# Kernel tuning notes

Measured on AMD Instinct MI355X. Metric: run time of the kernel, lower is better.

Reference implementation:

```python
import jax, jax.numpy as jnp
from jax import lax
import numpy as np
import math

B, L, D = 2, 1536, 1024
H = 8
C = 2 * D          # d_wide
DPH = C // H       # 256, dim_per_head
K = 4              # causal conv kernel size


def _ln(x, w, b=None, eps=1e-5):
    mu = jnp.mean(x, -1, keepdims=True)
    var = jnp.mean((x - mu) ** 2, -1, keepdims=True)
    y = (x - mu) * lax.rsqrt(var + eps) * w
    return y + b if b is not None else y


def setup_inputs() -> dict:
    key = jax.random.key(0)
    ks = jax.random.split(key, 8)
    x = jax.random.normal(ks[0], (B, L, D), jnp.float32)
    ln_w = jnp.ones((D,), jnp.float32)
    ln_b = jnp.zeros((D,), jnp.float32)
    w1 = jax.random.normal(ks[1], (4 * D, D), jnp.float32) * math.sqrt(2.0 / 5.0 / D)
    b1 = jnp.zeros((4 * D,), jnp.float32)
    conv_w = jax.random.normal(ks[2], (C, C, K), jnp.float32) * (1.0 / math.sqrt(C * K))
    conv_b = jnp.zeros((C,), jnp.float32)
    skip = jnp.ones((C,), jnp.float32)
    wqk = jax.random.normal(ks[3], (H, DPH, 2 * DPH), jnp.float32) * (1.0 / math.sqrt(DPH))
    bqk = jnp.zeros((H, 2 * DPH), jnp.float32)
    wv = jax.random.normal(ks[4], (H, DPH, DPH), jnp.float32) * (1.0 / math.sqrt(DPH))
    bv = jnp.zeros((H, DPH), jnp.float32)
    wif = jnp.zeros((2 * H, 3 * C), jnp.float32)  # zero-init per source
    bif = jnp.concatenate([jax.random.normal(ks[5], (H,), jnp.float32) * 0.1,
                           jnp.linspace(3.0, 6.0, H, dtype=jnp.float32)])
    hn_w = jnp.ones((DPH,), jnp.float32)
    w2 = jax.random.normal(ks[6], (D, C), jnp.float32) * (2.0 / 24.0 / math.sqrt(D))
    b2 = jnp.zeros((D,), jnp.float32)
    return {"x": x, "ln_w": ln_w, "ln_b": ln_b, "w1": w1, "b1": b1,
            "conv_w": conv_w, "conv_b": conv_b, "skip": skip,
            "wqk": wqk, "bqk": bqk, "wv": wv, "bv": bv,
            "wif": wif, "bif": bif, "hn_w": hn_w, "w2": w2, "b2": b2}


def _causal_conv(x1, conv_w, conv_b):
    # literal translation: permute(1,2,0), left-pad last dim, conv1d, permute(2,0,1)
    t = jnp.transpose(x1, (1, 2, 0))                  # (L, C, B)
    t = jnp.pad(t, ((0, 0), (0, 0), (K - 1, 0)))      # left pad along dim0 of original
    o = lax.conv_general_dilated(t, conv_w, (1,), 'VALID',
                                 dimension_numbers=('NCH', 'OIH', 'NCH'))
    o = o + conv_b[None, :, None]
    return jnp.transpose(o, (2, 0, 1))                # (B, L, C)


def _mlstm_core(qk, v_in, wqk, bqk, wv, bv, wif, bif, hn_w):
    b_, l_, c_ = qk.shape
    qkh = qk.reshape(b_, l_, H, DPH)
    proj = jnp.einsum('blhi,hio->blho', qkh, wqk) + bqk       # (B,L,H,2*DPH)
    q, k = jnp.split(proj, 2, axis=-1)                        # each (B,L,H,DPH)
    v = jnp.einsum('blhi,hio->blho', v_in.reshape(b_, l_, H, DPH), wv) + bv
    qkv = jnp.concatenate([proj, v], axis=-1).reshape(b_, l_, 3 * c_)
    gates = qkv @ wif.T + bif                                 # (B,L,2H)
    i_g, f_g = jnp.split(gates, 2, axis=-1)                   # (B,L,H)
    i_g = jnp.exp(i_g)
    f_c = jnp.cumsum(jax.nn.log_sigmoid(f_g), axis=1)
    fmat = f_c[:, :, None, :] - f_c[:, None, :, :]            # (B,o,i,H)
    mask = jnp.triu(jnp.ones((l_, l_), bool), 1)[None, :, :, None]
    fmat = jnp.where(mask, -jnp.inf, fmat)
    d = fmat + i_g[:, None, :, :]
    m = jnp.max(d, axis=-2, keepdims=True)                    # over i: (B,o,1,H)
    d = jnp.exp(d - m)
    ks_ = k / math.sqrt(DPH)
    c = jnp.einsum('bohd,bihd->boih', q, ks_) * d
    bsum = jnp.sum(c, axis=-2, keepdims=True)                 # (B,o,1,H)
    n = jnp.maximum(jnp.abs(bsum), jnp.exp(-m))
    c = c / n
    h = jnp.einsum('boih,bihd->bohd', c, v)                   # (B,L,H,DPH)
    h = _ln(h, hn_w)                                          # LayerNorm, no bias
    return h.reshape(b_, l_, c_)


def reference(x, ln_w, ln_b, w1, b1, conv_w, conv_b, skip, wqk, bqk, wv, bv,
              wif, bif, hn_w, w2, b2):
    y = _ln(x, ln_w, ln_b) @ w1.T + b1                        # (B,L,4D)
    x1, x2 = jnp.split(y, 2, axis=-1)                         # each (B,L,C)
    qk = jax.nn.silu(_causal_conv(x1, conv_w, conv_b))
    h = _mlstm_core(qk, x1, wqk, bqk, wv, bv, wif, bif, hn_w)
    x1o = h + skip * qk
    xm = x1o * jax.nn.silu(x2)
    return xm @ w2.T + b2 + x
```

## Files before the change

kernel.cpp:

```cpp
#include <hip/hip_runtime.h>

typedef unsigned short u16;
typedef __bf16 bf16x8 __attribute__((ext_vector_type(8)));
typedef float f32x4 __attribute__((ext_vector_type(4)));
typedef unsigned short us8 __attribute__((ext_vector_type(8)));

#define MFMA(a,b,c) __builtin_amdgcn_mfma_f32_16x16x32_bf16((a),(b),(c),0,0,0)
#define DEV __device__ __forceinline__

DEV u16 f2bf(float f){
  unsigned u = __float_as_uint(f);
  u += 0x7fffu + ((u >> 16) & 1u);
  return (u16)(u >> 16);
}
DEV float bf2f(u16 v){ return __uint_as_float(((unsigned)v)<<16); }
DEV float silu_f(float v){ return v / (1.f + __expf(-v)); }
DEV bf16x8 asbf(us8 v){ return __builtin_bit_cast(bf16x8, v); }

__global__ void prep_kernel(const float* __restrict__ w1, const float* __restrict__ w2,
                            const float* __restrict__ wif, const float* __restrict__ conv_w,
                            const float* __restrict__ wqk, const float* __restrict__ wv,
                            u16* __restrict__ w1b, u16* __restrict__ w2b, u16* __restrict__ wifb,
                            u16* __restrict__ cw2, u16* __restrict__ cw3,
                            u16* __restrict__ wqkt, u16* __restrict__ wvt)
{
  const long N0 = 4194304;
  const long N1 = N0 + 2097152;
  const long N2 = N1 + 98304;
  const long N3 = N2 + 4194304;
  const long N4 = N3 + 1048576;
  const long N5 = N4 + 524288;
  long stride = (long)gridDim.x * blockDim.x;
  for (long i = (long)blockIdx.x*blockDim.x + threadIdx.x; i < N5; i += stride) {
    if (i < N0)      { w1b[i] = f2bf(w1[i]); }
    else if (i < N1) { long j = i-N0; w2b[j] = f2bf(w2[j]); }
    else if (i < N2) { long j = i-N1; wifb[j] = f2bf(wif[j]); }
    else if (i < N3) { long j = i-N2; float2 t = *(const float2*)(conv_w + j*4 + 2);
                       cw2[j] = f2bf(t.x); cw3[j] = f2bf(t.y); }
    else if (i < N4) { long j = i-N3; long h=j>>17, r=j&131071, o=r>>8, ii=r&255;
                       wqkt[j] = f2bf(wqk[h*131072 + ii*512 + o]); }
    else             { long j = i-N4; long h=j>>16, o=(j>>8)&255, ii=j&255;
                       wvt[j] = f2bf(wv[h*65536 + ii*256 + o]); }
  }
}

__global__ __launch_bounds__(256) void ln_kernel(const float* __restrict__ x,
        const float* __restrict__ w, const float* __restrict__ b, u16* __restrict__ xn)
{
  int row = blockIdx.x, tid = threadIdx.x;
  const float* xr = x + (long)row*1024;
  float4 v = *(const float4*)(xr + tid*4);
  float s = v.x+v.y+v.z+v.w;
  float q = v.x*v.x+v.y*v.y+v.z*v.z+v.w*v.w;
  #pragma unroll
  for (int off=32; off>=1; off>>=1){ s += __shfl_xor(s,off); q += __shfl_xor(q,off); }
  __shared__ float red[8];
  int wv_ = tid>>6;
  if ((tid&63)==0){ red[wv_*2]=s; red[wv_*2+1]=q; }
  __syncthreads();
  s = red[0]+red[2]+red[4]+red[6];
  q = red[1]+red[3]+red[5]+red[7];
  float mu = s*(1.f/1024.f);
  float var = q*(1.f/1024.f) - mu*mu;
  float rs = rsqrtf(var + 1e-5f);
  int c = tid*4;
  u16 o0 = f2bf((v.x-mu)*rs*w[c+0] + b[c+0]);
  u16 o1 = f2bf((v.y-mu)*rs*w[c+1] + b[c+1]);
  u16 o2 = f2bf((v.z-mu)*rs*w[c+2] + b[c+2]);
  u16 o3 = f2bf((v.w-mu)*rs*w[c+3] + b[c+3]);
  uint2 pk;
  pk.x = (unsigned)o0 | ((unsigned)o1<<16);
  pk.y = (unsigned)o2 | ((unsigned)o3<<16);
  *(uint2*)(xn + (long)row*1024 + c) = pk;
}

__global__ __launch_bounds__(256,2) void gemm_bt(
    const u16* __restrict__ A, long lda, long sAz,
    const u16* __restrict__ A2,
    const u16* __restrict__ Bm, long ldb, long sBz,
    const u16* __restrict__ B2,
    int K1, int Ktot, int convmode,
    const float* __restrict__ bias, long sBiasz,
    int epi,
    float* __restrict__ outf, long ldo, long sOfz,
    u16* __restrict__ outb, long ldob, long sObz,
    const float* __restrict__ resid,
    float* __restrict__ outf2)
{
  __shared__ u16 AsF[4096];
  __shared__ u16 BsF[4096];
  int tid = threadIdx.x;
  int bz = blockIdx.z;
  A += (long)bz*sAz; Bm += (long)bz*sBz;
  const float* biasz = bias ? (bias + (long)bz*sBiasz) : bias;
  u16* outbz = outb ? (outb + (long)bz*sObz) : outb;
  float* outfz = outf ? (outf + (long)bz*sOfz) : outf;
  long am0 = (long)blockIdx.y*128;
  long bn0 = (long)blockIdx.x*128;
  int lane = tid&63, wave = tid>>6, quad = lane>>4, l15 = lane&15;
  int wm = wave>>1, wn = wave&1;
  int kq8 = quad*8;
  int dual = convmode && (bz==1);
  int Kt = dual ? Ktot : K1;
  f32x4 acc[4][4] = {};
  for (int k0=0; k0<Kt; k0+=32) {
    const u16* Ak; const u16* Bk; int kk;
    if (dual){
      if (k0 < K1){ Ak = A; Bk = B2; kk = k0; }
      else        { Ak = A2; Bk = Bm; kk = k0 - K1; }
    } else { Ak = A; Bk = Bm; kk = k0; }
    __syncthreads();
    __builtin_amdgcn_global_load_lds((const __attribute__((address_space(1))) void*)(Ak + (am0 + wave*16 + l15)*lda + kk + kq8),
                                     (__attribute__((address_space(3))) void*)(AsF + wave*512), 16, 0, 0);
    __builtin_amdgcn_global_load_lds((const __attribute__((address_space(1))) void*)(Ak + (am0 + (wave+4)*16 + l15)*lda + kk + kq8),
                                     (__attribute__((address_space(3))) void*)(AsF + (wave+4)*512), 16, 0, 0);
    __builtin_amdgcn_global_load_lds((const __attribute__((address_space(1))) void*)(Bk + (bn0 + wave*16 + l15)*ldb + kk + kq8),
                                     (__attribute__((address_space(3))) void*)(BsF + wave*512), 16, 0, 0);
    __builtin_amdgcn_global_load_lds((const __attribute__((address_space(1))) void*)(Bk + (bn0 + (wave+4)*16 + l15)*ldb + kk + kq8),
                                     (__attribute__((address_space(3))) void*)(BsF + (wave+4)*512), 16, 0, 0);
    __syncthreads();
    bf16x8 af[4], bfr[4];
    #pragma unroll
    for (int t=0;t<4;t++){
      af[t]  = *(const bf16x8*)&AsF[(wm*4+t)*512 + quad*128 + l15*8];
      bfr[t] = *(const bf16x8*)&BsF[(wn*4+t)*512 + quad*128 + l15*8];
    }
    #pragma unroll
    for (int ti=0;ti<4;ti++)
      #pragma unroll
      for (int tj=0;tj<4;tj++)
        acc[ti][tj] = MFMA(af[ti], bfr[tj], acc[ti][tj]);
  }
  #pragma unroll
  for (int ti=0;ti<4;ti++)
  #pragma unroll
  for (int tj=0;tj<4;tj++)
  #pragma unroll
  for (int r=0;r<4;r++){
    long m = am0 + wm*64 + ti*16 + quad*4 + r;
    long n = bn0 + wn*64 + tj*16 + l15;
    float v = acc[ti][tj][r];
    if (epi==1){ outbz[m*ldob+n] = f2bf(v + biasz[n]); }
    else if (epi==2){
      v += biasz[n];
      if (n < 2048) outbz[m*ldob+n] = f2bf(v);
      else outf2[m*2048 + n - 2048] = silu_f(v);
    }
    else if (epi==3){
      v += biasz[n]; v = silu_f(v);
      outfz[m*ldo+n] = v; outbz[m*ldob+n] = f2bf(v);
    }
    else { outfz[m*ldo+n] = v + biasz[n] + resid[m*1024+n]; }
  }
}

__global__ __launch_bounds__(256) void gates_gemm(const u16* __restrict__ qkv,
        const u16* __restrict__ wifb, float* __restrict__ gates)
{
  int tid = threadIdx.x;
  int lane = tid&63, wave = tid>>6, quad = lane>>4, l15 = lane&15;
  long m0 = (long)blockIdx.x*128 + wave*32;
  int ks = blockIdx.y*1536;
  const u16* arow = qkv + (m0 + l15)*6144;
  const u16* brow = wifb + (long)l15*6144;
  f32x4 acc[2] = {};
  for (int k0=ks; k0<ks+1536; k0+=32){
    bf16x8 a0 = *(const bf16x8*)(arow + k0 + quad*8);
    bf16x8 a1 = *(const bf16x8*)(arow + (long)16*6144 + k0 + quad*8);
    bf16x8 bb = *(const bf16x8*)(brow + k0 + quad*8);
    acc[0] = MFMA(a0,bb,acc[0]);
    acc[1] = MFMA(a1,bb,acc[1]);
  }
  #pragma unroll
  for (int mt=0;mt<2;mt++)
  #pragma unroll
  for (int r=0;r<4;r++)
    atomicAdd(&gates[(m0 + mt*16 + quad*4 + r)*16 + l15], acc[mt][r]);
}

__global__ void scan_kernel(const float* __restrict__ gates, const float* __restrict__ bif,
        float* __restrict__ g_arr, float* __restrict__ mg_arr, float* __restrict__ enm)
{
  int bh = blockIdx.x; int b = bh>>3, h = bh&7;
  int lane = threadIdx.x;
  float bi = bif[h], bff = bif[8+h];
  float fl[24], gl[24];
  int l0 = lane*24;
  float s = 0.f;
  #pragma unroll
  for (int j=0;j<24;j++){
    int l = l0+j;
    float f = gates[((long)(b*1536+l))*16 + 8 + h] + bff;
    float ls = fminf(f,0.f) - log1pf(expf(-fabsf(f)));
    fl[j] = ls; s += ls;
  }
  float tot = s;
  for (int off=1; off<64; off<<=1){ float t = __shfl_up(s, off); if (lane>=off) s += t; }
  float fc = s - tot;
  float lm = -INFINITY;
  #pragma unroll
  for (int j=0;j<24;j++){
    int l = l0+j;
    fc += fl[j];
    fl[j] = fc;
    float ir = gates[((long)(b*1536+l))*16 + h] + bi;
    float g = expf(ir) - fc;
    gl[j] = g;
    lm = fmaxf(lm, g);
  }
  float im = lm;
  for (int off=1; off<64; off<<=1){ float t = __shfl_up(im, off); if (lane>=off) im = fmaxf(im,t); }
  float ex = __shfl_up(im, 1);
  if (lane==0) ex = -INFINITY;
  float rm = ex;
  #pragma unroll
  for (int j=0;j<24;j++){
    rm = fmaxf(rm, gl[j]);
    long idx = (long)bh*1536 + l0 + j;
    g_arr[idx] = gl[j];
    mg_arr[idx] = rm;
    enm[idx] = expf(-(fl[j] + rm));
  }
}

__global__ __launch_bounds__(256) void repack_kernel(const u16* __restrict__ qkv,
        u16* __restrict__ qf, u16* __restrict__ kf, u16* __restrict__ vf)
{
  int bh = blockIdx.x, c = blockIdx.y;
  int b = bh>>3, h = bh&7;
  int tid = threadIdx.x;
  long rowb = (long)b*1536 + c*32;
  #pragma unroll
  for (int s4=0; s4<4; s4++){
    int s = s4*256 + tid;
    int n16 = s>>9, kc=(s>>6)&7, l=s&63, quad=l>>4, l15=l&15;
    const u16* src = qkv + (rowb + n16*16 + l15)*6144 + h*768 + kc*32 + quad*8;
    us8 q = *(const us8*)src;
    us8 k = *(const us8*)(src + 256);
    us8 ksc;
    #pragma unroll
    for (int j=0;j<8;j++) ksc[j] = f2bf(bf2f(k[j])*0.0625f);
    int tj = s>>6;
    us8 v;
    #pragma unroll
    for (int j=0;j<8;j++)
      v[j] = qkv[(rowb + quad*8 + j)*6144 + h*768 + 512 + tj*16 + l15];
    long dst = ((long)(bh*48+c))*8192 + (long)s*8;
    *(us8*)(qf+dst) = q;
    *(us8*)(kf+dst) = ksc;
    *(us8*)(vf+dst) = v;
  }
}

__global__ __launch_bounds__(256,2) void attn_kernel(
    const u16* __restrict__ qf, const u16* __restrict__ kf, const u16* __restrict__ vf,
    const float* __restrict__ g_arr, const float* __restrict__ mg_arr,
    const float* __restrict__ enm,
    const float* __restrict__ hn_w, const float* __restrict__ skip,
    const float* __restrict__ qkf, const float* __restrict__ s2,
    u16* __restrict__ xm)
{
  __shared__ u16 pl[4][32][40];
  __shared__ float red[256*36];
  __shared__ float redb[3][32];
  int tid = threadIdx.x;
  int lane = tid&63, wave = tid>>6, quad = lane>>4, l15 = lane&15;
  int bh = blockIdx.x, b = bh>>3, h = bh&7;
  int otile = 47 - blockIdx.y;
  int ow0 = otile*32;
  const u16* qfb = qf + ((long)(bh*48+otile))*8192;
  us8 qreg[2][8];
  #pragma unroll
  for (int mt=0;mt<2;mt++)
    #pragma unroll
    for (int kc=0;kc<8;kc++)
      qreg[mt][kc] = *(const us8*)(qfb + mt*4096 + kc*512 + lane*8);
  float mg[2][4];
  #pragma unroll
  for (int mt=0;mt<2;mt++)
    #pragma unroll
    for (int r=0;r<4;r++)
      mg[mt][r] = mg_arr[(long)bh*1536 + ow0 + mt*16 + quad*4 + r];
  f32x4 accv[2][16] = {};
  float bs[2][4] = {};
  for (int it=wave; it<=otile; it+=4){
    int i0 = it*32;
    const u16* kfb = kf + ((long)(bh*48+it))*8192;
    f32x4 sacc[2][2] = {};
    #pragma unroll
    for (int kc=0;kc<8;kc++){
      bf16x8 b0 = *(const bf16x8*)(kfb + kc*512 + lane*8);
      bf16x8 b1 = *(const bf16x8*)(kfb + 4096 + kc*512 + lane*8);
      sacc[0][0] = MFMA(asbf(qreg[0][kc]), b0, sacc[0][0]);
      sacc[0][1] = MFMA(asbf(qreg[0][kc]), b1, sacc[0][1]);
      sacc[1][0] = MFMA(asbf(qreg[1][kc]), b0, sacc[1][0]);
      sacc[1][1] = MFMA(asbf(qreg[1][kc]), b1, sacc[1][1]);
    }
    #pragma unroll
    for (int nt=0;nt<2;nt++){
      float gi = g_arr[(long)bh*1536 + i0 + nt*16 + l15];
      #pragma unroll
      for (int mt=0;mt<2;mt++)
        #pragma unroll
        for (int r=0;r<4;r++){
          int oi = ow0 + mt*16 + quad*4 + r;
          int ii = i0 + nt*16 + l15;
          float p = (ii <= oi) ? sacc[mt][nt][r]*__expf(gi - mg[mt][r]) : 0.f;
          bs[mt][r] += p;
          pl[wave][mt*16+quad*4+r][nt*16+l15] = f2bf(p);
        }
    }
    const u16* vfb = vf + ((long)(bh*48+it))*8192;
    bf16x8 pa0 = *(const bf16x8*)&pl[wave][l15][quad*8];
    bf16x8 pa1 = *(const bf16x8*)&pl[wave][16+l15][quad*8];
    #pragma unroll
    for (int tj=0;tj<16;tj++){
      bf16x8 vb = *(const bf16x8*)(vfb + tj*512 + lane*8);
      accv[0][tj] = MFMA(pa0, vb, accv[0][tj]);
      accv[1][tj] = MFMA(pa1, vb, accv[1][tj]);
    }
  }
  #pragma unroll
  for (int mt=0;mt<2;mt++)
    #pragma unroll
    for (int r=0;r<4;r++)
      #pragma unroll
      for (int off=1; off<16; off<<=1) bs[mt][r] += __shfl_xor(bs[mt][r], off);
  for (int w=1; w<4; w++){
    if (wave==w){
      #pragma unroll
      for (int mt=0;mt<2;mt++)
        #pragma unroll
        for (int tj=0;tj<16;tj++)
          *(f32x4*)&red[(tj*16+l15)*36 + mt*16 + quad*4] = accv[mt][tj];
      if (l15==0){
        #pragma unroll
        for (int mt=0;mt<2;mt++)
          #pragma unroll
          for (int r=0;r<4;r++)
            redb[w-1][mt*16+quad*4+r] = bs[mt][r];
      }
    }
    __syncthreads();
    if (wave==0){
      #pragma unroll
      for (int mt=0;mt<2;mt++)
        #pragma unroll
        for (int tj=0;tj<16;tj++)
          accv[mt][tj] += *(const f32x4*)&red[(tj*16+l15)*36 + mt*16 + quad*4];
      #pragma unroll
      for (int mt=0;mt<2;mt++)
        #pragma unroll
        for (int r=0;r<4;r++)
          bs[mt][r] += redb[w-1][mt*16+quad*4+r];
    }
    __syncthreads();
  }
  if (wave != 0) return;
  long browg = (long)b*1536;
  #pragma unroll
  for (int mt=0;mt<2;mt++){
    #pragma unroll
    for (int r=0;r<4;r++){
      int row = ow0 + mt*16 + quad*4 + r;
      float s1 = 0.f, sq = 0.f;
      #pragma unroll
      for (int tj=0;tj<16;tj++){ float a = accv[mt][tj][r]; s1 += a; sq += a*a; }
      #pragma unroll
      for (int off=1; off<16; off<<=1){ s1 += __shfl_xor(s1,off); sq += __shfl_xor(sq,off); }
      float nv = fmaxf(fabsf(bs[mt][r]), enm[(long)bh*1536 + row]);
      float inv = 1.f/nv;
      float mu = s1*inv*(1.f/256.f);
      float var = sq*inv*inv*(1.f/256.f) - mu*mu;
      float rs = rsqrtf(var + 1e-5f);
      long rg = browg + row;
      #pragma unroll
      for (int tj=0;tj<16;tj++){
        int col = tj*16 + l15;
        int cc = h*256 + col;
        float y = (accv[mt][tj][r]*inv - mu)*rs*hn_w[col];
        float xv = (y + skip[cc]*qkf[rg*2048 + cc]) * s2[rg*2048 + cc];
        xm[rg*2048 + cc] = f2bf(xv);
      }
    }
  }
}

extern "C" void kernel_launch(void* const* d_in, const int* in_sizes, int n_in,
                              void* d_out, int out_size, void* d_ws, size_t ws_size,
                              hipStream_t stream)
{
  const float* x      = (const float*)d_in[0];
  const float* ln_w   = (const float*)d_in[1];
  const float* ln_b   = (const float*)d_in[2];
  const float* w1     = (const float*)d_in[3];
  const float* b1     = (const float*)d_in[4];
  const float* conv_w = (const float*)d_in[5];
  const float* conv_b = (const float*)d_in[6];
  const float* skip   = (const float*)d_in[7];
  const float* wqk    = (const float*)d_in[8];
  const float* bqk    = (const float*)d_in[9];
  const float* wv     = (const float*)d_in[10];
  const float* bv     = (const float*)d_in[11];
  const float* wif    = (const float*)d_in[12];
  const float* bif    = (const float*)d_in[13];
  const float* hn_w   = (const float*)d_in[14];
  const float* w2     = (const float*)d_in[15];
  const float* b2     = (const float*)d_in[16];
  float* out = (float*)d_out;

  char* p = (char*)d_ws;
  auto alloc = [&](size_t bytes)->void*{ void* r = (void*)p; p += (bytes + 255) & ~(size_t)255; return r; };
  u16* w1b  = (u16*)alloc((size_t)4194304*2);
  u16* w2b  = (u16*)alloc((size_t)2097152*2);
  u16* wifb = (u16*)alloc((size_t)98304*2);
  u16* cw2  = (u16*)alloc((size_t)4194304*2);
  u16* cw3  = (u16*)alloc((size_t)4194304*2);
  u16* wqkt = (u16*)alloc((size_t)1048576*2);
  u16* wvt  = (u16*)alloc((size_t)524288*2);
  u16* xn   = (u16*)alloc((size_t)3072*1024*2);
  u16* x1b  = (u16*)alloc((size_t)3072*2048*2);
  float* s2 = (float*)alloc((size_t)3072*2048*4);
  float* qkf= (float*)alloc((size_t)3072*2048*4);
  u16* qkb  = (u16*)alloc((size_t)3072*2048*2);
  u16* qkv  = (u16*)alloc((size_t)3072*6144*2);
  u16* qfb  = (u16*)alloc((size_t)16*48*8192*2);
  u16* kfb  = (u16*)alloc((size_t)16*48*8192*2);
  u16* vfb  = (u16*)alloc((size_t)16*48*8192*2);
  float* gates = (float*)alloc((size_t)3072*16*4);
  float* g_arr = (float*)alloc((size_t)16*1536*4);
  float* mg_arr= (float*)alloc((size_t)16*1536*4);
  float* enm   = (float*)alloc((size_t)16*1536*4);
  u16* xmb  = (u16*)alloc((size_t)3072*2048*2);
  if ((size_t)(p - (char*)d_ws) > ws_size) return;

  hipMemsetAsync(gates, 0, (size_t)3072*16*4, stream);
  prep_kernel<<<4096, 256, 0, stream>>>(w1, w2, wif, conv_w, wqk, wv,
                                        w1b, w2b, wifb, cw2, cw3, wqkt, wvt);
  ln_kernel<<<3072, 256, 0, stream>>>(x, ln_w, ln_b, xn);
  gemm_bt<<<dim3(32,24,1), 256, 0, stream>>>(xn, 1024, 0, nullptr, w1b, 1024, 0, nullptr,
       1024, 1024, 0, b1, 0, 2, nullptr, 0, 0, x1b, 2048, 0, nullptr, s2);
  gemm_bt<<<dim3(16,12,2), 256, 0, stream>>>(x1b, 2048, 0, x1b + (long)1536*2048,
       cw3, 2048, 0, cw2, 2048, 4096, 1, conv_b, 0, 3,
       qkf, 2048, (long)1536*2048, qkb, 2048, (long)1536*2048, nullptr, nullptr);
  gemm_bt<<<dim3(4,24,8), 256, 0, stream>>>(qkb, 2048, 256, nullptr, wqkt, 256, 131072, nullptr,
       256, 256, 0, bqk, 512, 1, nullptr, 0, 0, qkv, 6144, 768, nullptr, nullptr);
  gemm_bt<<<dim3(2,24,8), 256, 0, stream>>>(x1b, 2048, 256, nullptr, wvt, 256, 65536, nullptr,
       256, 256, 0, bv, 256, 1, nullptr, 0, 0, qkv + 512, 6144, 768, nullptr, nullptr);
  repack_kernel<<<dim3(16,48,1), 256, 0, stream>>>(qkv, qfb, kfb, vfb);
  gates_gemm<<<dim3(24,4,1), 256, 0, stream>>>(qkv, wifb, gates);
  scan_kernel<<<16, 64, 0, stream>>>(gates, bif, g_arr, mg_arr, enm);
  attn_kernel<<<dim3(16,48,1), 256, 0, stream>>>(qfb, kfb, vfb, g_arr, mg_arr, enm,
       hn_w, skip, qkf, s2, xmb);
  gemm_bt<<<dim3(8,24,1), 256, 0, stream>>>(xmb, 2048, 0, nullptr, w2b, 2048, 0, nullptr,
       2048, 2048, 0, b2, 0, 4, out, 1024, 0, nullptr, 0, 0, x, nullptr);
}
```

Measured before the change: 653.1 us.

## Store GEMM operands in MFMA fragment-tiled layout and load directly to registers

Weights and activations feeding the GEMMs are now written by the prep, layernorm, conv-epilogue and attention kernels in a pre-swizzled fragment layout, so each wave can read its MFMA operands straight from global memory as contiguous 16-byte vectors. The new GEMM drops the LDS staging and both barriers per K step, prefetches the next K chunk into registers, and raises the occupancy hint to 3 blocks per CU. This removes LDS round-trips and synchronisation, but every wave now fetches its own operand tiles from global memory or cache with no sharing between waves through LDS. It also adds register pressure from the double-buffered fragments.

```diff
diff --git a/kernel.cpp b/kernel.cpp
--- a/kernel.cpp
+++ b/kernel.cpp
@@ -17,30 +17,69 @@
 DEV float silu_f(float v){ return v / (1.f + __expf(-v)); }
 DEV bf16x8 asbf(us8 v){ return __builtin_bit_cast(bf16x8, v); }
 
+DEV long fidxA(int m, int n, int KC){
+  return ((long)(m>>4)*KC + (n>>5))*512 + (((n>>3)&3)*16 + (m&15))*8 + (n&7);
+}
+DEV long fidxB(int n, int k0, int KC){
+  return ((long)((n>>6)*KC + (k0>>5)))*2048 + ((n>>4)&3)*512 + (((k0>>3)&3)*16 + (n&15))*8;
+}
+
 __global__ void prep_kernel(const float* __restrict__ w1, const float* __restrict__ w2,
                             const float* __restrict__ wif, const float* __restrict__ conv_w,
                             const float* __restrict__ wqk, const float* __restrict__ wv,
-                            u16* __restrict__ w1b, u16* __restrict__ w2b, u16* __restrict__ wifb,
-                            u16* __restrict__ cw2, u16* __restrict__ cw3,
-                            u16* __restrict__ wqkt, u16* __restrict__ wvt)
-{
-  const long N0 = 4194304;
-  const long N1 = N0 + 2097152;
-  const long N2 = N1 + 98304;
-  const long N3 = N2 + 4194304;
-  const long N4 = N3 + 1048576;
-  const long N5 = N4 + 524288;
+                            u16* __restrict__ w1f, u16* __restrict__ w2f, u16* __restrict__ wifb,
+                            u16* __restrict__ cw2f, u16* __restrict__ cw3f,
+                            u16* __restrict__ wqkf, u16* __restrict__ wvf)
+{
+  const long G0 = 524288;
+  const long G1 = G0 + 262144;
+  const long G2 = G1 + 524288;
+  const long G3 = G2 + 131072;
+  const long G4 = G3 + 65536;
+  const long G5 = G4 + 12288;
   long stride = (long)gridDim.x * blockDim.x;
-  for (long i = (long)blockIdx.x*blockDim.x + threadIdx.x; i < N5; i += stride) {
-    if (i < N0)      { w1b[i] = f2bf(w1[i]); }
-    else if (i < N1) { long j = i-N0; w2b[j] = f2bf(w2[j]); }
-    else if (i < N2) { long j = i-N1; wifb[j] = f2bf(wif[j]); }
-    else if (i < N3) { long j = i-N2; float2 t = *(const float2*)(conv_w + j*4 + 2);
-                       cw2[j] = f2bf(t.x); cw3[j] = f2bf(t.y); }
-    else if (i < N4) { long j = i-N3; long h=j>>17, r=j&131071, o=r>>8, ii=r&255;
-                       wqkt[j] = f2bf(wqk[h*131072 + ii*512 + o]); }
-    else             { long j = i-N4; long h=j>>16, o=(j>>8)&255, ii=j&255;
-                       wvt[j] = f2bf(wv[h*65536 + ii*256 + o]); }
+  for (long g = (long)blockIdx.x*blockDim.x + threadIdx.x; g < G5; g += stride) {
+    if (g < G0){
+      int n = (int)(g>>7), k0 = ((int)g&127)*8;
+      us8 o;
+      #pragma unroll
+      for (int j=0;j<8;j++) o[j] = f2bf(w1[(long)n*1024 + k0 + j]);
+      *(us8*)(w1f + fidxB(n,k0,32)) = o;
+    } else if (g < G1){
+      long r = g-G0; int n = (int)(r>>8), k0 = ((int)r&255)*8;
+      us8 o;
+      #pragma unroll
+      for (int j=0;j<8;j++) o[j] = f2bf(w2[(long)n*2048 + k0 + j]);
+      *(us8*)(w2f + fidxB(n,k0,64)) = o;
+    } else if (g < G2){
+      long r = g-G1; int n = (int)(r>>8), k0 = ((int)r&255)*8;
+      us8 o2, o3;
+      #pragma unroll
+      for (int j=0;j<8;j++){
+        float2 t = *(const float2*)(conv_w + ((long)n*2048 + k0 + j)*4 + 2);
+        o2[j] = f2bf(t.x); o3[j] = f2bf(t.y);
+      }
+      long fi = fidxB(n,k0,64);
+      *(us8*)(cw2f + fi) = o2; *(us8*)(cw3f + fi) = o3;
+    } else if (g < G3){
+      long r = g-G2; int h = (int)(r>>14); int q = (int)(r&16383);
+      int n = q>>5, k0 = (q&31)*8;
+      us8 o;
+      #pragma unroll
+      for (int j=0;j<8;j++) o[j] = f2bf(wqk[(long)h*131072 + (long)(k0+j)*512 + n]);
+      *(us8*)(wqkf + (long)h*131072 + fidxB(n,k0,8)) = o;
+    } else if (g < G4){
+      long r = g-G3; int h = (int)(r>>13); int q = (int)(r&8191);
+      int n = q>>5, k0 = (q&31)*8;
+      us8 o;
+      #pragma unroll
+      for (int j=0;j<8;j++) o[j] = f2bf(wv[(long)h*65536 + (long)(k0+j)*256 + n]);
+      *(us8*)(wvf + (long)h*65536 + fidxB(n,k0,8)) = o;
+    } else {
+      long r = (g-G4)*8;
+      #pragma unroll
+      for (int j=0;j<8;j++) wifb[r+j] = f2bf(wif[r+j]);
+    }
   }
 }
 
@@ -71,15 +110,16 @@
   uint2 pk;
   pk.x = (unsigned)o0 | ((unsigned)o1<<16);
   pk.y = (unsigned)o2 | ((unsigned)o3<<16);
-  *(uint2*)(xn + (long)row*1024 + c) = pk;
-}
-
-__global__ __launch_bounds__(256,2) void gemm_bt(
-    const u16* __restrict__ A, long lda, long sAz,
-    const u16* __restrict__ A2,
-    const u16* __restrict__ Bm, long ldb, long sBz,
-    const u16* __restrict__ B2,
-    int K1, int Ktot, int convmode,
+  long fi = ((long)(row>>4)*32 + (tid>>3))*512 + (((tid>>1)&3)*16 + (row&15))*8 + (tid&1)*4;
+  *(uint2*)(xn + fi) = pk;
+}
+
+__global__ __launch_bounds__(256,3) void rgemm(
+    const u16* __restrict__ Af, int aKC, long sAz,
+    const u16* __restrict__ A2f,
+    const u16* __restrict__ Bf, int bKC, long sBz,
+    const u16* __restrict__ B2f,
+    int k1, int ktot, int convmode,
     const float* __restrict__ bias, long sBiasz,
     int epi,
     float* __restrict__ outf, long ldo, long sOfz,
@@ -87,70 +127,73 @@
     const float* __restrict__ resid,
     float* __restrict__ outf2)
 {
-  __shared__ u16 AsF[4096];
-  __shared__ u16 BsF[4096];
-  int tid = threadIdx.x;
-  int bz = blockIdx.z;
-  A += (long)bz*sAz; Bm += (long)bz*sBz;
-  const float* biasz = bias ? (bias + (long)bz*sBiasz) : bias;
-  u16* outbz = outb ? (outb + (long)bz*sObz) : outb;
-  float* outfz = outf ? (outf + (long)bz*sOfz) : outf;
-  long am0 = (long)blockIdx.y*128;
-  long bn0 = (long)blockIdx.x*128;
+  int tid = threadIdx.x, bz = blockIdx.z;
   int lane = tid&63, wave = tid>>6, quad = lane>>4, l15 = lane&15;
   int wm = wave>>1, wn = wave&1;
-  int kq8 = quad*8;
+  const u16* A = Af + bz*sAz;
+  const u16* B = Bf + bz*sBz;
+  const float* biasz = bias ? bias + bz*sBiasz : nullptr;
+  u16* outbz = outb ? outb + bz*sObz : nullptr;
+  float* outfz = outf ? outf + bz*sOfz : nullptr;
+  int am0 = blockIdx.y*128, bn0 = blockIdx.x*128;
   int dual = convmode && (bz==1);
-  int Kt = dual ? Ktot : K1;
+  long aRow0 = (long)(am0>>4) + wm*4;
+  long bN64  = (long)(bn0>>6) + wn;
   f32x4 acc[4][4] = {};
-  for (int k0=0; k0<Kt; k0+=32) {
-    const u16* Ak; const u16* Bk; int kk;
-    if (dual){
-      if (k0 < K1){ Ak = A; Bk = B2; kk = k0; }
-      else        { Ak = A2; Bk = Bm; kk = k0 - K1; }
-    } else { Ak = A; Bk = Bm; kk = k0; }
-    __syncthreads();
-    __builtin_amdgcn_global_load_lds((const __attribute__((address_space(1))) void*)(Ak + (am0 + wave*16 + l15)*lda + kk + kq8),
-                                     (__attribute__((address_space(3))) void*)(AsF + wave*512), 16, 0, 0);
-    __builtin_amdgcn_global_load_lds((const __attribute__((address_space(1))) void*)(Ak + (am0 + (wave+4)*16 + l15)*lda + kk + kq8),
-                                     (__attribute__((address_space(3))) void*)(AsF + (wave+4)*512), 16, 0, 0);
-    __builtin_amdgcn_global_load_lds((const __attribute__((address_space(1))) void*)(Bk + (bn0 + wave*16 + l15)*ldb + kk + kq8),
-                                     (__attribute__((address_space(3))) void*)(BsF + wave*512), 16, 0, 0);
-    __builtin_amdgcn_global_load_lds((const __attribute__((address_space(1))) void*)(Bk + (bn0 + (wave+4)*16 + l15)*ldb + kk + kq8),
-                                     (__attribute__((address_space(3))) void*)(BsF + (wave+4)*512), 16, 0, 0);
-    __syncthreads();
-    bf16x8 af[4], bfr[4];
+  auto runseg = [&](const u16* As, const u16* Bs, int cnt){
+    const u16* ap[4]; const u16* bp[4];
     #pragma unroll
     for (int t=0;t<4;t++){
-      af[t]  = *(const bf16x8*)&AsF[(wm*4+t)*512 + quad*128 + l15*8];
-      bfr[t] = *(const bf16x8*)&BsF[(wn*4+t)*512 + quad*128 + l15*8];
-    }
-    #pragma unroll
-    for (int ti=0;ti<4;ti++)
-      #pragma unroll
-      for (int tj=0;tj<4;tj++)
-        acc[ti][tj] = MFMA(af[ti], bfr[tj], acc[ti][tj]);
-  }
+      ap[t] = As + (aRow0 + t)*aKC*512 + lane*8;
+      bp[t] = Bs + bN64*bKC*2048 + t*512 + lane*8;
+    }
+    bf16x8 a[4], b[4], an[4], bn[4];
+    #pragma unroll
+    for (int t=0;t<4;t++){
+      a[t] = *(const bf16x8*)(ap[t]);
+      b[t] = *(const bf16x8*)(bp[t]);
+    }
+    #pragma unroll 2
+    for (int kc=0; kc<cnt; kc++){
+      if (kc+1 < cnt){
+        #pragma unroll
+        for (int t=0;t<4;t++){
+          an[t] = *(const bf16x8*)(ap[t] + (long)(kc+1)*512);
+          bn[t] = *(const bf16x8*)(bp[t] + (long)(kc+1)*2048);
+        }
+      }
+      #pragma unroll
+      for (int ti=0;ti<4;ti++)
+        #pragma unroll
+        for (int tj=0;tj<4;tj++)
+          acc[ti][tj] = MFMA(a[ti], b[tj], acc[ti][tj]);
+      #pragma unroll
+      for (int t=0;t<4;t++){ a[t]=an[t]; b[t]=bn[t]; }
+    }
+  };
+  if (dual){ runseg(Af, B2f, k1); runseg(A2f, Bf, ktot - k1); }
+  else     { runseg(A, B, k1); }
   #pragma unroll
   for (int ti=0;ti<4;ti++)
   #pragma unroll
   for (int tj=0;tj<4;tj++)
   #pragma unroll
   for (int r=0;r<4;r++){
-    long m = am0 + wm*64 + ti*16 + quad*4 + r;
-    long n = bn0 + wn*64 + tj*16 + l15;
+    int m = am0 + wm*64 + ti*16 + quad*4 + r;
+    int n = bn0 + wn*64 + tj*16 + l15;
     float v = acc[ti][tj][r];
-    if (epi==1){ outbz[m*ldob+n] = f2bf(v + biasz[n]); }
+    if (epi==1){ outbz[(long)m*ldob + n] = f2bf(v + biasz[n]); }
     else if (epi==2){
       v += biasz[n];
-      if (n < 2048) outbz[m*ldob+n] = f2bf(v);
-      else outf2[m*2048 + n - 2048] = silu_f(v);
+      if (n < 2048) outbz[fidxA(m,n,64)] = f2bf(v);
+      else outf2[(long)m*2048 + n - 2048] = silu_f(v);
     }
     else if (epi==3){
-      v += biasz[n]; v = silu_f(v);
-      outfz[m*ldo+n] = v; outbz[m*ldob+n] = f2bf(v);
-    }
-    else { outfz[m*ldo+n] = v + biasz[n] + resid[m*1024+n]; }
+      v = silu_f(v + biasz[n]);
+      outfz[(long)m*ldo + n] = v;
+      outbz[fidxA(m,n,64)] = f2bf(v);
+    }
+    else { outfz[(long)m*ldo + n] = v + biasz[n] + resid[(long)m*1024 + n]; }
   }
 }
 
@@ -380,7 +423,7 @@
         int cc = h*256 + col;
         float y = (accv[mt][tj][r]*inv - mu)*rs*hn_w[col];
         float xv = (y + skip[cc]*qkf[rg*2048 + cc]) * s2[rg*2048 + cc];
-        xm[rg*2048 + cc] = f2bf(xv);
+        xm[((long)(rg>>4)*64 + (cc>>5))*512 + (((cc>>3)&3)*16 + (row&15))*8 + (cc&7)] = f2bf(xv);
       }
     }
   }
@@ -411,18 +454,18 @@
 
   char* p = (char*)d_ws;
   auto alloc = [&](size_t bytes)->void*{ void* r = (void*)p; p += (bytes + 255) & ~(size_t)255; return r; };
-  u16* w1b  = (u16*)alloc((size_t)4194304*2);
-  u16* w2b  = (u16*)alloc((size_t)2097152*2);
+  u16* w1f  = (u16*)alloc((size_t)4194304*2);
+  u16* w2f  = (u16*)alloc((size_t)2097152*2);
   u16* wifb = (u16*)alloc((size_t)98304*2);
-  u16* cw2  = (u16*)alloc((size_t)4194304*2);
-  u16* cw3  = (u16*)alloc((size_t)4194304*2);
-  u16* wqkt = (u16*)alloc((size_t)1048576*2);
-  u16* wvt  = (u16*)alloc((size_t)524288*2);
-  u16* xn   = (u16*)alloc((size_t)3072*1024*2);
-  u16* x1b  = (u16*)alloc((size_t)3072*2048*2);
+  u16* cw2f = (u16*)alloc((size_t)4194304*2);
+  u16* cw3f = (u16*)alloc((size_t)4194304*2);
+  u16* wqkf = (u16*)alloc((size_t)1048576*2);
+  u16* wvf  = (u16*)alloc((size_t)524288*2);
+  u16* xnf  = (u16*)alloc((size_t)3072*1024*2);
+  u16* x1bf = (u16*)alloc((size_t)3072*2048*2);
   float* s2 = (float*)alloc((size_t)3072*2048*4);
   float* qkf= (float*)alloc((size_t)3072*2048*4);
-  u16* qkb  = (u16*)alloc((size_t)3072*2048*2);
+  u16* qkbf = (u16*)alloc((size_t)3072*2048*2);
   u16* qkv  = (u16*)alloc((size_t)3072*6144*2);
   u16* qfb  = (u16*)alloc((size_t)16*48*8192*2);
   u16* kfb  = (u16*)alloc((size_t)16*48*8192*2);
@@ -431,27 +474,27 @@
   float* g_arr = (float*)alloc((size_t)16*1536*4);
   float* mg_arr= (float*)alloc((size_t)16*1536*4);
   float* enm   = (float*)alloc((size_t)16*1536*4);
-  u16* xmb  = (u16*)alloc((size_t)3072*2048*2);
+  u16* xmf  = (u16*)alloc((size_t)3072*2048*2);
   if ((size_t)(p - (char*)d_ws) > ws_size) return;
 
   hipMemsetAsync(gates, 0, (size_t)3072*16*4, stream);
   prep_kernel<<<4096, 256, 0, stream>>>(w1, w2, wif, conv_w, wqk, wv,
-                                        w1b, w2b, wifb, cw2, cw3, wqkt, wvt);
-  ln_kernel<<<3072, 256, 0, stream>>>(x, ln_w, ln_b, xn);
-  gemm_bt<<<dim3(32,24,1), 256, 0, stream>>>(xn, 1024, 0, nullptr, w1b, 1024, 0, nullptr,
-       1024, 1024, 0, b1, 0, 2, nullptr, 0, 0, x1b, 2048, 0, nullptr, s2);
-  gemm_bt<<<dim3(16,12,2), 256, 0, stream>>>(x1b, 2048, 0, x1b + (long)1536*2048,
-       cw3, 2048, 0, cw2, 2048, 4096, 1, conv_b, 0, 3,
-       qkf, 2048, (long)1536*2048, qkb, 2048, (long)1536*2048, nullptr, nullptr);
-  gemm_bt<<<dim3(4,24,8), 256, 0, stream>>>(qkb, 2048, 256, nullptr, wqkt, 256, 131072, nullptr,
-       256, 256, 0, bqk, 512, 1, nullptr, 0, 0, qkv, 6144, 768, nullptr, nullptr);
-  gemm_bt<<<dim3(2,24,8), 256, 0, stream>>>(x1b, 2048, 256, nullptr, wvt, 256, 65536, nullptr,
-       256, 256, 0, bv, 256, 1, nullptr, 0, 0, qkv + 512, 6144, 768, nullptr, nullptr);
+                                        w1f, w2f, wifb, cw2f, cw3f, wqkf, wvf);
+  ln_kernel<<<3072, 256, 0, stream>>>(x, ln_w, ln_b, xnf);
+  rgemm<<<dim3(32,24,1), 256, 0, stream>>>(xnf, 32, 0, nullptr, w1f, 32, 0, nullptr,
+       32, 32, 0, b1, 0, 2, nullptr, 0, 0, x1bf, 0, 0, nullptr, s2);
+  rgemm<<<dim3(16,12,2), 256, 0, stream>>>(x1bf, 64, 0, x1bf + (long)96*64*512,
+       cw3f, 64, 0, cw2f, 64, 128, 1, conv_b, 0, 3,
+       qkf, 2048, (long)1536*2048, qkbf, 0, (long)96*64*512, nullptr, nullptr);
+  rgemm<<<dim3(4,24,8), 256, 0, stream>>>(qkbf, 64, 4096, nullptr, wqkf, 8, 131072, nullptr,
+       8, 8, 0, bqk, 512, 1, nullptr, 0, 0, qkv, 6144, 768, nullptr, nullptr);
+  rgemm<<<dim3(2,24,8), 256, 0, stream>>>(x1bf, 64, 4096, nullptr, wvf, 8, 65536, nullptr,
+       8, 8, 0, bv, 256, 1, nullptr, 0, 0, qkv + 512, 6144, 768, nullptr, nullptr);
   repack_kernel<<<dim3(16,48,1), 256, 0, stream>>>(qkv, qfb, kfb, vfb);
   gates_gemm<<<dim3(24,4,1), 256, 0, stream>>>(qkv, wifb, gates);
   scan_kernel<<<16, 64, 0, stream>>>(gates, bif, g_arr, mg_arr, enm);
   attn_kernel<<<dim3(16,48,1), 256, 0, stream>>>(qfb, kfb, vfb, g_arr, mg_arr, enm,
-       hn_w, skip, qkf, s2, xmb);
-  gemm_bt<<<dim3(8,24,1), 256, 0, stream>>>(xmb, 2048, 0, nullptr, w2b, 2048, 0, nullptr,
-       2048, 2048, 0, b2, 0, 4, out, 1024, 0, nullptr, 0, 0, x, nullptr);
-}
+       hn_w, skip, qkf, s2, xmf);
+  rgemm<<<dim3(8,24,1), 256, 0, stream>>>(xmf, 64, 0, nullptr, w2f, 64, 0, nullptr,
+       64, 64, 0, b2, 0, 4, out, 1024, 0, nullptr, 0, 0, x, nullptr);
+}
```

New measurement: 690.6 us. +5.8%, slower.
